# Optimization experiments

Hardware: AMD Instinct MI355X
Metric: run time of the kernel (lower is better)

The kernel has to match this reference:

```python
import jax, jax.numpy as jnp
import numpy as np


def _conv1x1(x, W, b):
    # x: (B,C,H,W), W: (O,C), b: (O,)
    return jnp.einsum('bchw,oc->bohw', x, W) + b[None, :, None, None]


def _maxpool2(x):
    B, C, H, W = x.shape
    return x.reshape(B, C, H // 2, 2, W // 2, 2).max(axis=(3, 5))


def setup_inputs() -> dict:
    key = jax.random.key(0)
    ks = jax.random.split(key, 6)
    B, C, H, W = 8, 1024, 64, 64
    DI, DO = 512, 1024
    std = 0.01  # matches nn.init.normal_(std=0.01)
    return {
        'x': jax.random.normal(ks[0], (B, C, H, W), dtype=jnp.float32),
        'W_theta': std * jax.random.normal(ks[1], (DI, C), dtype=jnp.float32),
        'b_theta': jnp.zeros((DI,), jnp.float32),
        'W_phi': std * jax.random.normal(ks[2], (DI, C), dtype=jnp.float32),
        'b_phi': jnp.zeros((DI,), jnp.float32),
        'W_g': std * jax.random.normal(ks[3], (DI, C), dtype=jnp.float32),
        'b_g': jnp.zeros((DI,), jnp.float32),
        'W_out': std * jax.random.normal(ks[4], (DO, DI), dtype=jnp.float32),
        'b_out': jnp.zeros((DO,), jnp.float32),
    }


def reference(x, W_theta, b_theta, W_phi, b_phi, W_g, b_g, W_out, b_out):
    B, C, H, W = x.shape
    di = W_theta.shape[0]
    scale = di ** (-0.5)
    # queries from full-res map: (B, di, N) with N = H*W
    theta = _conv1x1(x, W_theta, b_theta).reshape(B, di, H * W)
    # keys/values from 2x2-maxpooled map: (B, di, M), M = (H/2)*(W/2)
    px = _maxpool2(x)
    phi = _conv1x1(px, W_phi, b_phi).reshape(B, di, -1)
    g = _conv1x1(px, W_g, b_g).reshape(B, di, -1)
    # attention: (B, N, M)
    logits = jnp.einsum('bdn,bdm->bnm', theta, phi) * scale
    p = jax.nn.softmax(logits, axis=-1)
    # aggregate values: (B, di, N) -> (B, di, H, W)
    t = jnp.einsum('bdm,bnm->bdn', g, p).reshape(B, di, H, W)
    y = _conv1x1(t, W_out, b_out)
    return y + x
```

## Files before the change

kernel.cpp:

```cpp
#include <hip/hip_runtime.h>
#include <hip/hip_bf16.h>
#include <stdint.h>

typedef __bf16 bf16;
typedef __bf16 bf16x8 __attribute__((ext_vector_type(8)));
typedef __bf16 bf16x4 __attribute__((ext_vector_type(4)));
typedef float f32x4 __attribute__((ext_vector_type(4)));

#define GLOAD_LDS16(gptr, lptr)                                                        \
  __builtin_amdgcn_global_load_lds((const __attribute__((address_space(1))) void*)(gptr), \
                                   (__attribute__((address_space(3))) void*)(lptr), 16, 0, 0)

__global__ __launch_bounds__(256) void cast_f2b(const float* __restrict__ in,
                                                bf16* __restrict__ out, int n) {
  int i = (blockIdx.x * 256 + threadIdx.x) * 4;
  if (i >= n) return;
  const float4 v = *(const float4*)(in + i);
  bf16x4 o;
  o[0] = (bf16)v.x; o[1] = (bf16)v.y; o[2] = (bf16)v.z; o[3] = (bf16)v.w;
  *(bf16x4*)(out + i) = o;
}

__global__ __launch_bounds__(256) void zero_k(float* __restrict__ p, int n) {
  int i = blockIdx.x * 256 + threadIdx.x;
  if (i < n) p[i] = 0.f;
}

__global__ __launch_bounds__(256) void concat512(const float* __restrict__ a,
                                                 const float* __restrict__ b,
                                                 float* __restrict__ o) {
  int i = blockIdx.x * 256 + threadIdx.x;
  if (i < 512) o[i] = a[i];
  else if (i < 1024) o[i] = b[i - 512];
}

__global__ __launch_bounds__(256) void prep_kernel(const float* __restrict__ x,
                                                   bf16* __restrict__ xbT,
                                                   bf16* __restrict__ pxT) {
  const int b = blockIdx.y;
  x   += (size_t)b * 1024 * 4096;
  xbT += (size_t)b * 4096 * 1024;
  pxT += (size_t)b * 1024 * 1024;
  const int bid = blockIdx.x;
  const int h0 = bid & 31, ct = bid >> 5;
  const int tid = threadIdx.x;
  __shared__ float tile[64][129];
  const float* xs = x + (size_t)(ct * 64) * 4096 + h0 * 128;
#pragma unroll
  for (int e = 0; e < 8; ++e) {
    const int idx = e * 256 + tid;
    const int c = idx >> 5, n4 = (idx & 31) * 4;
    *(float4*)&tile[c][n4] = *(const float4*)&xs[(size_t)c * 4096 + n4];
  }
  __syncthreads();
  bf16* xo = xbT + (size_t)(h0 * 128) * 1024 + ct * 64;
#pragma unroll
  for (int e = 0; e < 4; ++e) {
    const int flat = e * 256 + tid;
    const int n = flat >> 3, c8 = (flat & 7) * 8;
    bf16x8 o;
#pragma unroll
    for (int j = 0; j < 8; ++j) o[j] = (bf16)tile[c8 + j][n];
    *(bf16x8*)&xo[(size_t)n * 1024 + c8] = o;
  }
  bf16* po = pxT + (size_t)(h0 * 32) * 1024 + ct * 64;
  {
    const int m = tid >> 3, c8 = (tid & 7) * 8;
    bf16x8 o;
#pragma unroll
    for (int j = 0; j < 8; ++j) {
      const int c = c8 + j;
      float v = fmaxf(fmaxf(tile[c][2 * m], tile[c][2 * m + 1]),
                      fmaxf(tile[c][64 + 2 * m], tile[c][64 + 2 * m + 1]));
      o[j] = (bf16)v;
    }
    *(bf16x8*)&po[(size_t)m * 1024 + c8] = o;
  }
}

template <int EPI>
__global__ __launch_bounds__(512, 4) void gemm256(
    const bf16* __restrict__ A, long long sA, int lda,
    const bf16* __restrict__ B, long long sB, int ldb,
    void* __restrict__ Cv, long long sC, int ldc, int K,
    const float* __restrict__ bias,
    const float* __restrict__ resid, long long sResid, float scale,
    float* __restrict__ rs_out, int gx, int gy) {
  const int nwg = gridDim.x;
  const int flat = blockIdx.x;
  const int swz = (flat & 7) * (nwg >> 3) + (flat >> 3);
  const int bx = swz % gx;
  const int tmp = swz / gx;
  const int by = tmp % gy;
  const int z = tmp / gy;

  A += (size_t)z * sA;
  B += (size_t)z * sB;
  const int tid = threadIdx.x;
  const int w = tid >> 6, lane = tid & 63;
  const int r16 = lane & 15, q4 = lane >> 4;
  const int wm = w >> 2, wn = w & 3;
  const long long tileM = (long long)bx * 128;
  const long long tileN = (long long)by * 256;

  __shared__ bf16 As[2][4096];
  __shared__ bf16 Bs[2][8192];

  f32x4 acc[4][4] = {};

  const int srow = tid >> 2;
  const int skb  = (tid & 3) ^ ((srow >> 1) & 3);
  const char* Ag = (const char*)A + ((size_t)(tileM + srow) * lda + skb * 8) * 2;
  const char* Bg = (const char*)B + ((size_t)(tileN + srow) * ldb + skb * 8) * 2;
  const size_t b128 = (size_t)128 * ldb * 2;

  auto stage = [&](int T) {
    const int sl = T & 1;
    GLOAD_LDS16(Ag + (size_t)T * 64, &As[sl][w * 512]);
    GLOAD_LDS16(Bg + (size_t)T * 64, &Bs[sl][w * 512]);
    GLOAD_LDS16(Bg + (size_t)T * 64 + b128, &Bs[sl][4096 + w * 512]);
  };

  stage(0);
  const int NT = K >> 5;

  for (int T = 0; T < NT; ++T) {
    asm volatile("s_waitcnt vmcnt(0)" ::: "memory");
    __builtin_amdgcn_s_barrier();
    asm volatile("" ::: "memory");
    if (T + 1 < NT) stage(T + 1);

    const char* Asl = (const char*)&As[T & 1][0];
    const char* Bsl = (const char*)&Bs[T & 1][0];
    bf16x8 af[4], bf_[4];
#pragma unroll
    for (int mi = 0; mi < 4; ++mi) {
      const int row = wm * 64 + mi * 16 + r16;
      af[mi] = *(const bf16x8*)(Asl + row * 64 + ((q4 ^ ((row >> 1) & 3)) << 4));
    }
#pragma unroll
    for (int ni = 0; ni < 4; ++ni) {
      const int row = wn * 64 + ni * 16 + r16;
      bf_[ni] = *(const bf16x8*)(Bsl + row * 64 + ((q4 ^ ((row >> 1) & 3)) << 4));
    }
    __builtin_amdgcn_s_setprio(1);
#pragma unroll
    for (int mi = 0; mi < 4; ++mi)
#pragma unroll
      for (int ni = 0; ni < 4; ++ni)
        acc[mi][ni] = __builtin_amdgcn_mfma_f32_16x16x32_bf16(af[mi], bf_[ni], acc[mi][ni], 0, 0, 0);
    __builtin_amdgcn_s_setprio(0);
  }

  if constexpr (EPI == 4) {
    float* C = (float*)Cv + (size_t)z * sC;
    const float* rz = resid + (size_t)z * sResid;
#pragma unroll
    for (int a = 0; a < 4; ++a) {
      const int row0 = (int)tileM + wm * 64 + a * 16 + q4 * 4;
#pragma unroll
      for (int ni = 0; ni < 4; ++ni) {
        const int col = (int)tileN + wn * 64 + ni * 16 + r16;
#pragma unroll
        for (int r = 0; r < 4; ++r)
          C[(size_t)(row0 + r) * ldc + col] =
              acc[a][ni][r] + bias[row0 + r] + rz[(size_t)(row0 + r) * ldc + col];
      }
    }
  } else if constexpr (EPI == 8) {
    float* C = (float*)Cv + (size_t)z * sC;
    const float* rz = resid + (size_t)z * sResid;
    const float* rsp = rs_out + (size_t)z * 4096;
#pragma unroll
    for (int a = 0; a < 4; ++a) {
      const int row0 = (int)tileM + wm * 64 + a * 16 + q4 * 4;
      float bv[4];
#pragma unroll
      for (int r = 0; r < 4; ++r) bv[r] = bias[row0 + r];
#pragma unroll
      for (int ni = 0; ni < 4; ++ni) {
        const int col = (int)tileN + wn * 64 + ni * 16 + r16;
        const float cinv = 1.0f / rsp[col];
#pragma unroll
        for (int r = 0; r < 4; ++r)
          C[(size_t)(row0 + r) * ldc + col] =
              acc[a][ni][r] * cinv + bv[r] + rz[(size_t)(row0 + r) * ldc + col];
      }
    }
  } else if constexpr (EPI == 5) {
    bf16* C = (bf16*)Cv + (size_t)z * sC;
    float* rsp = rs_out + (size_t)z * 4096;
#pragma unroll
    for (int a = 0; a < 4; ++a) {
      const int row0 = (int)tileM + wm * 64 + a * 16 + q4 * 4;
      float psum[4] = {0.f, 0.f, 0.f, 0.f};
#pragma unroll
      for (int ni = 0; ni < 4; ++ni) {
        const int col = (int)tileN + wn * 64 + ni * 16 + r16;
#pragma unroll
        for (int r = 0; r < 4; ++r) {
          float e = __expf(acc[a][ni][r]);
          psum[r] += e;
          C[(size_t)(row0 + r) * ldc + col] = (bf16)e;
        }
      }
#pragma unroll
      for (int r = 0; r < 4; ++r) {
        float v = psum[r];
        v += __shfl_xor(v, 1);
        v += __shfl_xor(v, 2);
        v += __shfl_xor(v, 4);
        v += __shfl_xor(v, 8);
        if (r16 == 0) atomicAdd(&rsp[row0 + r], v);
      }
    }
  } else if constexpr (EPI == 7) {
    bf16* C = (bf16*)Cv + (size_t)z * sC;
    const float* rsp = bias + (size_t)z * 4096;
#pragma unroll
    for (int a = 0; a < 4; ++a) {
      const int row0 = (int)tileM + wm * 64 + a * 16 + q4 * 4;
      float inv[4];
#pragma unroll
      for (int r = 0; r < 4; ++r) inv[r] = 1.0f / rsp[row0 + r];
#pragma unroll
      for (int ni = 0; ni < 4; ++ni) {
        const int col = (int)tileN + wn * 64 + ni * 16 + r16;
#pragma unroll
        for (int r = 0; r < 4; ++r)
          C[(size_t)(row0 + r) * ldc + col] = (bf16)(acc[a][ni][r] * inv[r]);
      }
    }
  } else if constexpr (EPI == 2) {
    bf16* C = (bf16*)Cv + (size_t)z * sC;
#pragma unroll
    for (int a = 0; a < 4; ++a) {
      const int row0 = (int)tileM + wm * 64 + a * 16 + q4 * 4;
#pragma unroll
      for (int ni = 0; ni < 4; ++ni) {
        const int col = (int)tileN + wn * 64 + ni * 16 + r16;
#pragma unroll
        for (int r = 0; r < 4; ++r)
          C[(size_t)(row0 + r) * ldc + col] = (bf16)(acc[a][ni][r] + bias[row0 + r]);
      }
    }
  } else if constexpr (EPI == 0) {
    bf16* C = (bf16*)Cv + (size_t)z * sC;
#pragma unroll
    for (int a = 0; a < 4; ++a) {
      const int row0 = (int)tileM + wm * 64 + a * 16 + q4 * 4;
#pragma unroll
      for (int ni = 0; ni < 4; ++ni) {
        const int col = (int)tileN + wn * 64 + ni * 16 + r16;
#pragma unroll
        for (int r = 0; r < 4; ++r)
          C[(size_t)(row0 + r) * ldc + col] = (bf16)acc[a][ni][r];
      }
    }
  } else {
    bf16* C = (bf16*)Cv + (size_t)z * sC;
#pragma unroll
    for (int a = 0; a < 4; ++a) {
      const int row0 = (int)tileM + wm * 64 + a * 16 + q4 * 4;
#pragma unroll
      for (int ni = 0; ni < 4; ++ni) {
        const int col = (int)tileN + wn * 64 + ni * 16 + r16;
        const float badd = bias[col];
#pragma unroll
        for (int r = 0; r < 4; ++r)
          C[(size_t)(row0 + r) * ldc + col] = (bf16)((acc[a][ni][r] + badd) * scale);
      }
    }
  }
}

extern "C" void kernel_launch(void* const* d_in, const int* in_sizes, int n_in,
                              void* d_out, int out_size, void* d_ws, size_t ws_size,
                              hipStream_t stream) {
  const float* x  = (const float*)d_in[0];
  const float* Wt = (const float*)d_in[1];
  const float* bt = (const float*)d_in[2];
  const float* Wp = (const float*)d_in[3];
  const float* bp = (const float*)d_in[4];
  const float* Wg = (const float*)d_in[5];
  const float* bg = (const float*)d_in[6];
  const float* Wo = (const float*)d_in[7];
  const float* bo = (const float*)d_in[8];
  float* out = (float*)d_out;

  const size_t MB = 1024ull * 1024ull;
  char* ws = (char*)d_ws;
  bf16* WtB  = (bf16*)(ws + 0 * MB);
  bf16* WoB  = (bf16*)(ws + 1 * MB);
  bf16* WpgB = (bf16*)(ws + 2 * MB);

  cast_f2b<<<512, 256, 0, stream>>>(Wt, WtB, 512 * 1024);
  cast_f2b<<<512, 256, 0, stream>>>(Wo, WoB, 1024 * 512);
  cast_f2b<<<512, 256, 0, stream>>>(Wp, WpgB, 512 * 1024);
  cast_f2b<<<512, 256, 0, stream>>>(Wg, WpgB + 512 * 1024, 512 * 1024);

  const float SCALE = 0.044194173824159216f;

#define G256(EPI_, gx_, gy_, gz_, A_, sA_, lda_, B_, sB_, ldb_, Cv_, sC_, ldc_, K_, \
             bias_, resid_, sResid_, scale_, rs_)                                    \
  gemm256<EPI_><<<(gx_) * (gy_) * (gz_), 512, 0, stream>>>(                          \
      A_, sA_, lda_, B_, sB_, ldb_, Cv_, sC_, ldc_, K_, bias_, resid_, sResid_,      \
      scale_, rs_, gx_, gy_)

  if (ws_size >= 164 * MB) {
    float* bias_pg = (float*)(ws + 4 * MB);
    float* rsum    = (float*)(ws + 4 * MB + 65536);
    bf16* pxT    = (bf16*)(ws + 5 * MB);
    bf16* pg     = (bf16*)(ws + 21 * MB);
    bf16* thetaT = (bf16*)(ws + 37 * MB);
    bf16* W2     = (bf16*)(ws + 69 * MB);
    bf16* xbT    = (bf16*)(ws + 100 * MB);
    bf16* Pt     = xbT;

    concat512<<<4, 256, 0, stream>>>(bp, bg, bias_pg);
    prep_kernel<<<dim3(512, 8), 256, 0, stream>>>(x, xbT, pxT);
    G256(1, 32, 2, 8, xbT, 4096ll * 1024, 1024, WtB, 0, 1024,
         thetaT, 4096ll * 512, 512, 1024, bt, nullptr, 0, SCALE, nullptr);
    G256(1, 8, 4, 8, pxT, 1024ll * 1024, 1024, WpgB, 0, 1024,
         pg, 1024ll * 1024, 1024, 1024, bias_pg, nullptr, 0, 1.f, nullptr);
    G256(0, 8, 4, 8, WoB, 0, 512, pg + 512, 1024ll * 1024, 1024,
         W2, 1024ll * 1024, 1024, 512, nullptr, nullptr, 0, 1.f, nullptr);
    zero_k<<<128, 256, 0, stream>>>(rsum, 32768);
    G256(5, 32, 4, 8, thetaT, 4096ll * 512, 512, pg, 1024ll * 1024, 1024,
         Pt, 4096ll * 1024, 1024, 512, nullptr, nullptr, 0, 1.f, rsum);
    G256(8, 8, 16, 8, W2, 1024ll * 1024, 1024, Pt, 4096ll * 1024, 1024,
         out, 1024ll * 4096, 4096, 1024, bo, x, 1024ll * 4096, 1.f, rsum);
  } else if (ws_size >= 108 * MB) {
    bf16* WpB = WpgB;
    bf16* WgB = WpgB + 512 * 1024;
    bf16* pxT    = (bf16*)(ws + 4 * MB);
    bf16* phiT   = (bf16*)(ws + 20 * MB);
    bf16* g      = (bf16*)(ws + 28 * MB);
    bf16* thetaT = (bf16*)(ws + 36 * MB);
    bf16* tT     = (bf16*)(ws + 68 * MB);
    bf16* xbT    = (bf16*)(ws + 100 * MB);
    float* rsum = (float*)((char*)d_out + 80 * MB);
    for (int b = 0; b < 8; ++b) {
      prep_kernel<<<dim3(512, 1), 256, 0, stream>>>(x + (size_t)b * 1024 * 4096, xbT,
                                                    pxT + (size_t)b * 1024 * 1024);
      G256(1, 32, 2, 1, xbT, 0, 1024, WtB, 0, 1024,
           thetaT + (size_t)b * 4096 * 512, 0, 512, 1024, bt, nullptr, 0, SCALE, nullptr);
    }
    G256(1, 8, 2, 8, pxT, 1024ll * 1024, 1024, WpB, 0, 1024,
         phiT, 1024ll * 512, 512, 1024, bp, nullptr, 0, 1.f, nullptr);
    G256(2, 4, 4, 8, WgB, 0, 1024, pxT, 1024ll * 1024, 1024,
         g, 512ll * 1024, 1024, 1024, bg, nullptr, 0, 1.f, nullptr);
    for (int b = 0; b < 8; ++b) {
      bf16* Ptb = (bf16*)d_out + (size_t)b * 4096 * 1024;
      zero_k<<<16, 256, 0, stream>>>(rsum + (size_t)b * 4096, 4096);
      G256(5, 32, 4, 1, thetaT + (size_t)b * 4096 * 512, 0, 512,
           phiT + (size_t)b * 1024 * 512, 0, 512,
           Ptb, 0, 1024, 512, nullptr, nullptr, 0, 1.f, rsum + (size_t)b * 4096);
      G256(7, 32, 2, 1, Ptb, 0, 1024, g + (size_t)b * 512 * 1024, 0, 1024,
           tT + (size_t)b * 4096 * 512, 0, 512, 1024,
           rsum + (size_t)b * 4096, nullptr, 0, 1.f, nullptr);
    }
    G256(4, 8, 16, 8, WoB, 0, 512, tT, 4096ll * 512, 512,
         out, 1024ll * 4096, 4096, 512, bo, x, 1024ll * 4096, 1.f, nullptr);
  } else {
    bf16* WpB = WpgB;
    bf16* WgB = WpgB + 512 * 1024;
    float* rsum  = (float*)(ws + 4 * MB);
    bf16* pxT    = (bf16*)(ws + 5 * MB);
    bf16* phiT   = (bf16*)(ws + 7 * MB);
    bf16* g      = (bf16*)(ws + 8 * MB);
    bf16* thetaT = (bf16*)(ws + 9 * MB);
    bf16* tT     = (bf16*)(ws + 13 * MB);
    bf16* Pt     = (bf16*)(ws + 17 * MB);
    bf16* xbT    = (bf16*)(ws + 25 * MB);
    for (int b = 0; b < 8; ++b) {
      prep_kernel<<<dim3(512, 1), 256, 0, stream>>>(x + (size_t)b * 1024 * 4096, xbT, pxT);
      G256(1, 32, 2, 1, xbT, 0, 1024, WtB, 0, 1024,
           thetaT, 0, 512, 1024, bt, nullptr, 0, SCALE, nullptr);
      G256(1, 8, 2, 1, pxT, 0, 1024, WpB, 0, 1024,
           phiT, 0, 512, 1024, bp, nullptr, 0, 1.f, nullptr);
      G256(2, 4, 4, 1, WgB, 0, 1024, pxT, 0, 1024,
           g, 0, 1024, 1024, bg, nullptr, 0, 1.f, nullptr);
      zero_k<<<16, 256, 0, stream>>>(rsum, 4096);
      G256(5, 32, 4, 1, thetaT, 0, 512, phiT, 0, 512,
           Pt, 0, 1024, 512, nullptr, nullptr, 0, 1.f, rsum);
      G256(7, 32, 2, 1, Pt, 0, 1024, g, 0, 1024,
           tT, 0, 512, 1024, rsum, nullptr, 0, 1.f, nullptr);
      G256(4, 8, 16, 1, WoB, 0, 512, tT, 0, 512,
           out + (size_t)b * 1024 * 4096, 1024ll * 4096, 4096, 512,
           bo, x + (size_t)b * 1024 * 4096, 1024ll * 4096, 1.f, nullptr);
    }
  }
#undef G256
}
```

Before: 305.7 us.

## Add 256x256-tile GEMM with 8-phase interleaved load/MFMA schedule

Adds a new gemm8p kernel with 256x256 output tiles (8x4 accumulator fragments per wave), double-buffered LDS, and loads for the next K-step spread over four barrier-separated phases between MFMA groups. All five GEMMs in the large-workspace path now use it, with grid dims halved along M. The aim is more data reuse per tile and better overlap of global-to-LDS loads with compute. In exchange it needs 128KB of LDS and many more accumulator registers, which lowers occupancy (launch bound 2), and the grids get smaller, which can cause tail or under-fill effects on the GPU.

```diff
diff --git a/kernel.cpp b/kernel.cpp
--- a/kernel.cpp
+++ b/kernel.cpp
@@ -75,6 +75,184 @@
       o[j] = (bf16)v;
     }
     *(bf16x8*)&po[(size_t)m * 1024 + c8] = o;
+  }
+}
+
+template <int EPI>
+__global__ __launch_bounds__(512, 2) void gemm8p(
+    const bf16* __restrict__ A, long long sA, int lda,
+    const bf16* __restrict__ B, long long sB, int ldb,
+    void* __restrict__ Cv, long long sC, int ldc, int K,
+    const float* __restrict__ bias,
+    const float* __restrict__ resid, long long sResid, float scale,
+    float* __restrict__ rs_out, int gx, int gy) {
+  const int nwg = gridDim.x;
+  const int flat = blockIdx.x;
+  const int swz = (flat & 7) * (nwg >> 3) + (flat >> 3);
+  const int bx = swz % gx;
+  const int tmp = swz / gx;
+  const int by = tmp % gy;
+  const int z = tmp / gy;
+
+  A += (size_t)z * sA;
+  B += (size_t)z * sB;
+  const int tid = threadIdx.x;
+  const int w = tid >> 6, lane = tid & 63;
+  const int r16 = lane & 15, q4 = lane >> 4;
+  const int wm = w >> 2, wn = w & 3;
+  const long long tileM = (long long)bx * 256;
+  const long long tileN = (long long)by * 256;
+
+  __shared__ bf16 As[2][16384];
+  __shared__ bf16 Bs[2][16384];
+
+  f32x4 acc[8][4] = {};
+
+  const int trow = tid >> 3;
+  const int gsl  = (tid & 7) ^ (trow & 7);
+  const char* Ag = (const char*)A + ((size_t)(tileM + trow) * lda + gsl * 8) * 2;
+  const char* Bg = (const char*)B + ((size_t)(tileN + trow) * ldb + gsl * 8) * 2;
+
+  auto stg = [&](int S, int o) {
+    const int sl = S & 1;
+    if (o < 4)
+      GLOAD_LDS16(Ag + ((size_t)S * 64 + (size_t)o * 64 * lda) * 2,
+                  &As[sl][o * 4096 + w * 512]);
+    else
+      GLOAD_LDS16(Bg + ((size_t)S * 64 + (size_t)(o - 4) * 64 * ldb) * 2,
+                  &Bs[sl][(o - 4) * 4096 + w * 512]);
+  };
+
+  const int NT = K >> 6;
+#pragma unroll
+  for (int o = 0; o < 8; ++o) stg(0, o);
+
+  for (int T = 0; T < NT; ++T) {
+    const char* Asl = (const char*)&As[T & 1][0];
+    const char* Bsl = (const char*)&Bs[T & 1][0];
+    bf16x8 af[4], bf0[4], bf1[4];
+
+    auto rdA = [&](int h, int kk) {
+#pragma unroll
+      for (int mi = 0; mi < 4; ++mi) {
+        const int row = wm * 128 + h * 64 + mi * 16 + r16;
+        af[mi] = *(const bf16x8*)(Asl + row * 128 + (((kk * 4 + q4) ^ (row & 7)) << 4));
+      }
+    };
+    auto rdB = [&](bf16x8* bf, int kk) {
+#pragma unroll
+      for (int ni = 0; ni < 4; ++ni) {
+        const int row = wn * 64 + ni * 16 + r16;
+        bf[ni] = *(const bf16x8*)(Bsl + row * 128 + (((kk * 4 + q4) ^ (row & 7)) << 4));
+      }
+    };
+    auto mfma16 = [&](int h, bf16x8* bf) {
+      __builtin_amdgcn_s_setprio(1);
+#pragma unroll
+      for (int mi = 0; mi < 4; ++mi)
+#pragma unroll
+        for (int ni = 0; ni < 4; ++ni)
+          acc[h * 4 + mi][ni] =
+              __builtin_amdgcn_mfma_f32_16x16x32_bf16(af[mi], bf[ni], acc[h * 4 + mi][ni], 0, 0, 0);
+      __builtin_amdgcn_s_setprio(0);
+    };
+
+    asm volatile("s_waitcnt vmcnt(0)" ::: "memory");
+    __builtin_amdgcn_s_barrier();
+    asm volatile("" ::: "memory");
+    if (T + 1 < NT) { stg(T + 1, 0); stg(T + 1, 1); stg(T + 1, 2); }
+    rdA(0, 0); rdB(bf0, 0);
+    mfma16(0, bf0);
+    __builtin_amdgcn_s_barrier();
+    asm volatile("" ::: "memory");
+    if (T + 1 < NT) { stg(T + 1, 3); stg(T + 1, 4); stg(T + 1, 5); }
+    rdA(0, 1); rdB(bf1, 1);
+    mfma16(0, bf1);
+    __builtin_amdgcn_s_barrier();
+    asm volatile("" ::: "memory");
+    if (T + 1 < NT) { stg(T + 1, 6); stg(T + 1, 7); }
+    rdA(1, 0);
+    mfma16(1, bf0);
+    __builtin_amdgcn_s_barrier();
+    asm volatile("" ::: "memory");
+    rdA(1, 1);
+    mfma16(1, bf1);
+  }
+
+  if constexpr (EPI == 8) {
+    float* C = (float*)Cv + (size_t)z * sC;
+    const float* rz = resid + (size_t)z * sResid;
+    const float* rsp = rs_out + (size_t)z * 4096;
+#pragma unroll
+    for (int a = 0; a < 8; ++a) {
+      const int row0 = (int)tileM + wm * 128 + a * 16 + q4 * 4;
+      float bv[4];
+#pragma unroll
+      for (int r = 0; r < 4; ++r) bv[r] = bias[row0 + r];
+#pragma unroll
+      for (int ni = 0; ni < 4; ++ni) {
+        const int col = (int)tileN + wn * 64 + ni * 16 + r16;
+        const float cinv = 1.0f / rsp[col];
+#pragma unroll
+        for (int r = 0; r < 4; ++r)
+          C[(size_t)(row0 + r) * ldc + col] =
+              acc[a][ni][r] * cinv + bv[r] + rz[(size_t)(row0 + r) * ldc + col];
+      }
+    }
+  } else if constexpr (EPI == 5) {
+    bf16* C = (bf16*)Cv + (size_t)z * sC;
+    float* rsp = rs_out + (size_t)z * 4096;
+#pragma unroll
+    for (int a = 0; a < 8; ++a) {
+      const int row0 = (int)tileM + wm * 128 + a * 16 + q4 * 4;
+      float psum[4] = {0.f, 0.f, 0.f, 0.f};
+#pragma unroll
+      for (int ni = 0; ni < 4; ++ni) {
+        const int col = (int)tileN + wn * 64 + ni * 16 + r16;
+#pragma unroll
+        for (int r = 0; r < 4; ++r) {
+          float e = __expf(acc[a][ni][r]);
+          psum[r] += e;
+          C[(size_t)(row0 + r) * ldc + col] = (bf16)e;
+        }
+      }
+#pragma unroll
+      for (int r = 0; r < 4; ++r) {
+        float v = psum[r];
+        v += __shfl_xor(v, 1);
+        v += __shfl_xor(v, 2);
+        v += __shfl_xor(v, 4);
+        v += __shfl_xor(v, 8);
+        if (r16 == 0) atomicAdd(&rsp[row0 + r], v);
+      }
+    }
+  } else if constexpr (EPI == 0) {
+    bf16* C = (bf16*)Cv + (size_t)z * sC;
+#pragma unroll
+    for (int a = 0; a < 8; ++a) {
+      const int row0 = (int)tileM + wm * 128 + a * 16 + q4 * 4;
+#pragma unroll
+      for (int ni = 0; ni < 4; ++ni) {
+        const int col = (int)tileN + wn * 64 + ni * 16 + r16;
+#pragma unroll
+        for (int r = 0; r < 4; ++r)
+          C[(size_t)(row0 + r) * ldc + col] = (bf16)acc[a][ni][r];
+      }
+    }
+  } else {
+    bf16* C = (bf16*)Cv + (size_t)z * sC;
+#pragma unroll
+    for (int a = 0; a < 8; ++a) {
+      const int row0 = (int)tileM + wm * 128 + a * 16 + q4 * 4;
+#pragma unroll
+      for (int ni = 0; ni < 4; ++ni) {
+        const int col = (int)tileN + wn * 64 + ni * 16 + r16;
+        const float badd = bias[col];
+#pragma unroll
+        for (int r = 0; r < 4; ++r)
+          C[(size_t)(row0 + r) * ldc + col] = (bf16)((acc[a][ni][r] + badd) * scale);
+      }
+    }
   }
 }
 
@@ -167,26 +345,6 @@
               acc[a][ni][r] + bias[row0 + r] + rz[(size_t)(row0 + r) * ldc + col];
       }
     }
-  } else if constexpr (EPI == 8) {
-    float* C = (float*)Cv + (size_t)z * sC;
-    const float* rz = resid + (size_t)z * sResid;
-    const float* rsp = rs_out + (size_t)z * 4096;
-#pragma unroll
-    for (int a = 0; a < 4; ++a) {
-      const int row0 = (int)tileM + wm * 64 + a * 16 + q4 * 4;
-      float bv[4];
-#pragma unroll
-      for (int r = 0; r < 4; ++r) bv[r] = bias[row0 + r];
-#pragma unroll
-      for (int ni = 0; ni < 4; ++ni) {
-        const int col = (int)tileN + wn * 64 + ni * 16 + r16;
-        const float cinv = 1.0f / rsp[col];
-#pragma unroll
-        for (int r = 0; r < 4; ++r)
-          C[(size_t)(row0 + r) * ldc + col] =
-              acc[a][ni][r] * cinv + bv[r] + rz[(size_t)(row0 + r) * ldc + col];
-      }
-    }
   } else if constexpr (EPI == 5) {
     bf16* C = (bf16*)Cv + (size_t)z * sC;
     float* rsp = rs_out + (size_t)z * 4096;
@@ -242,19 +400,6 @@
 #pragma unroll
         for (int r = 0; r < 4; ++r)
           C[(size_t)(row0 + r) * ldc + col] = (bf16)(acc[a][ni][r] + bias[row0 + r]);
-      }
-    }
-  } else if constexpr (EPI == 0) {
-    bf16* C = (bf16*)Cv + (size_t)z * sC;
-#pragma unroll
-    for (int a = 0; a < 4; ++a) {
-      const int row0 = (int)tileM + wm * 64 + a * 16 + q4 * 4;
-#pragma unroll
-      for (int ni = 0; ni < 4; ++ni) {
-        const int col = (int)tileN + wn * 64 + ni * 16 + r16;
-#pragma unroll
-        for (int r = 0; r < 4; ++r)
-          C[(size_t)(row0 + r) * ldc + col] = (bf16)acc[a][ni][r];
       }
     }
   } else {
@@ -301,6 +446,11 @@
 
   const float SCALE = 0.044194173824159216f;
 
+#define G8P(EPI_, gx_, gy_, gz_, A_, sA_, lda_, B_, sB_, ldb_, Cv_, sC_, ldc_, K_,  \
+            bias_, resid_, sResid_, scale_, rs_)                                     \
+  gemm8p<EPI_><<<(gx_) * (gy_) * (gz_), 512, 0, stream>>>(                           \
+      A_, sA_, lda_, B_, sB_, ldb_, Cv_, sC_, ldc_, K_, bias_, resid_, sResid_,      \
+      scale_, rs_, gx_, gy_)
 #define G256(EPI_, gx_, gy_, gz_, A_, sA_, lda_, B_, sB_, ldb_, Cv_, sC_, ldc_, K_, \
              bias_, resid_, sResid_, scale_, rs_)                                    \
   gemm256<EPI_><<<(gx_) * (gy_) * (gz_), 512, 0, stream>>>(                          \
@@ -319,17 +469,17 @@
 
     concat512<<<4, 256, 0, stream>>>(bp, bg, bias_pg);
     prep_kernel<<<dim3(512, 8), 256, 0, stream>>>(x, xbT, pxT);
-    G256(1, 32, 2, 8, xbT, 4096ll * 1024, 1024, WtB, 0, 1024,
-         thetaT, 4096ll * 512, 512, 1024, bt, nullptr, 0, SCALE, nullptr);
-    G256(1, 8, 4, 8, pxT, 1024ll * 1024, 1024, WpgB, 0, 1024,
-         pg, 1024ll * 1024, 1024, 1024, bias_pg, nullptr, 0, 1.f, nullptr);
-    G256(0, 8, 4, 8, WoB, 0, 512, pg + 512, 1024ll * 1024, 1024,
-         W2, 1024ll * 1024, 1024, 512, nullptr, nullptr, 0, 1.f, nullptr);
+    G8P(1, 16, 2, 8, xbT, 4096ll * 1024, 1024, WtB, 0, 1024,
+        thetaT, 4096ll * 512, 512, 1024, bt, nullptr, 0, SCALE, nullptr);
+    G8P(1, 4, 4, 8, pxT, 1024ll * 1024, 1024, WpgB, 0, 1024,
+        pg, 1024ll * 1024, 1024, 1024, bias_pg, nullptr, 0, 1.f, nullptr);
+    G8P(0, 4, 4, 8, WoB, 0, 512, pg + 512, 1024ll * 1024, 1024,
+        W2, 1024ll * 1024, 1024, 512, nullptr, nullptr, 0, 1.f, nullptr);
     zero_k<<<128, 256, 0, stream>>>(rsum, 32768);
-    G256(5, 32, 4, 8, thetaT, 4096ll * 512, 512, pg, 1024ll * 1024, 1024,
-         Pt, 4096ll * 1024, 1024, 512, nullptr, nullptr, 0, 1.f, rsum);
-    G256(8, 8, 16, 8, W2, 1024ll * 1024, 1024, Pt, 4096ll * 1024, 1024,
-         out, 1024ll * 4096, 4096, 1024, bo, x, 1024ll * 4096, 1.f, rsum);
+    G8P(5, 16, 4, 8, thetaT, 4096ll * 512, 512, pg, 1024ll * 1024, 1024,
+        Pt, 4096ll * 1024, 1024, 512, nullptr, nullptr, 0, 1.f, rsum);
+    G8P(8, 4, 16, 8, W2, 1024ll * 1024, 1024, Pt, 4096ll * 1024, 1024,
+        out, 1024ll * 4096, 4096, 1024, bo, x, 1024ll * 4096, 1.f, rsum);
   } else if (ws_size >= 108 * MB) {
     bf16* WpB = WpgB;
     bf16* WgB = WpgB + 512 * 1024;
@@ -391,5 +541,6 @@
            bo, x + (size_t)b * 1024 * 4096, 1024ll * 4096, 1.f, nullptr);
     }
   }
+#undef G8P
 #undef G256
 }
```

New measurement: 351.8 us. +15.1%, slower.
